# Kernel tuning notes

Hardware: AMD Instinct MI355X
Metric: run time of the kernel (lower is better)

The kernel has to match this reference:

```python
import jax, jax.numpy as jnp
import numpy as np

B, N, C = 2, 3136, 256
NUM_HEADS = 8
RADIUS = 3.0


def spatial_mask(H, W, radius):
    # [N, 2] pixel coordinates, then pairwise Euclidean distance mask
    yy, xx = jnp.meshgrid(jnp.arange(H), jnp.arange(W), indexing='ij')
    coords = jnp.stack([yy, xx], axis=-1).astype(jnp.float32).reshape(-1, 2)
    d2 = jnp.sum((coords[:, None, :] - coords[None, :, :]) ** 2, axis=-1)
    return jnp.where(d2 > radius * radius, -jnp.inf, 0.0)  # [N, N]


def setup_inputs() -> dict:
    key = jax.random.key(0)
    ks = jax.random.split(key, 7)
    w = 0.02
    return {
        'x': jax.random.normal(ks[0], (B, N, C), jnp.float32),
        'x_kv': jax.random.normal(ks[1], (B, N, C), jnp.float32),
        'Wq': jax.random.normal(ks[2], (C, C), jnp.float32) * w,
        'Wk': jax.random.normal(ks[3], (C, C), jnp.float32) * w,
        'Wv': jax.random.normal(ks[4], (C, C), jnp.float32) * w,
        'Wp': jax.random.normal(ks[5], (C, C), jnp.float32) * w,
        'bp': jnp.zeros((C,), jnp.float32),
    }


def reference(x, x_kv, Wq, Wk, Wv, Wp, bp):
    Bc, Nc, Cc = x.shape
    H = W = int(Nc ** 0.5)
    hd = Cc // NUM_HEADS
    scale = hd ** (-0.5)
    # torch Linear: y = x @ W.T ; split heads -> [B, h, N, hd]
    q = (x @ Wq.T).reshape(Bc, Nc, NUM_HEADS, hd).transpose(0, 2, 1, 3)
    k = (x_kv @ Wk.T).reshape(Bc, Nc, NUM_HEADS, hd).transpose(0, 2, 1, 3)
    v = (x_kv @ Wv.T).reshape(Bc, Nc, NUM_HEADS, hd).transpose(0, 2, 1, 3)
    attn = jnp.einsum('bhnd,bhmd->bhnm', q, k) * scale
    attn = attn + spatial_mask(H, W, RADIUS)[None, None, :, :]
    attn = jax.nn.softmax(attn, axis=-1)
    out = jnp.einsum('bhnm,bhmd->bhnd', attn, v)
    out = out.transpose(0, 2, 1, 3).reshape(Bc, Nc, Cc)
    return out @ Wp.T + bp
```

## Files before the change

### kernel.cpp

```cpp
#include <hip/hip_runtime.h>


typedef float  f32x4  __attribute__((ext_vector_type(4)));
typedef __bf16 bf16x8 __attribute__((ext_vector_type(8)));
typedef unsigned short u16x4 __attribute__((ext_vector_type(4)));
typedef unsigned short u16x8 __attribute__((ext_vector_type(8)));

#define Nn    3136
#define Cc    256
#define Mrows 6272
#define BNC   1605632
#define GRID56 56

__device__ __forceinline__ unsigned short f2bf(float f) {
    unsigned u = __builtin_bit_cast(unsigned, f);
    u += 0x7fffu + ((u >> 16) & 1u);
    return (unsigned short)(u >> 16);
}
__device__ __forceinline__ float bf2f(unsigned short h) {
    unsigned u = (unsigned)h << 16;
    return __builtin_bit_cast(float, u);
}

template<bool A_BF16, bool OUT_BF16>
__device__ __forceinline__ void gemm_body(
    const void* __restrict__ Ap, const float* __restrict__ W,
    const float* __restrict__ bias, void* __restrict__ Yv,
    int m0, int n0)
{
    constexpr int LDSW = 72;
    __shared__ unsigned short lA[64 * LDSW];
    __shared__ unsigned short lB[64 * LDSW];

    const int t    = threadIdx.x;
    const int lane = t & 63;
    const int wave = t >> 6;
    const int wm   = wave >> 1;
    const int wn   = wave & 1;
    const int srow = t >> 2;
    const int scol = (t & 3) * 16;
    const int fr   = lane & 15;
    const int fk   = (lane >> 4) * 8;

    f32x4 acc[2][2] = {};

    for (int k0 = 0; k0 < 256; k0 += 64) {
        u16x8 astage[2], bstage[2];
        if constexpr (A_BF16) {
            const unsigned short* A = (const unsigned short*)Ap;
            astage[0] = *reinterpret_cast<const u16x8*>(A + (size_t)(m0 + srow) * 256 + k0 + scol);
            astage[1] = *reinterpret_cast<const u16x8*>(A + (size_t)(m0 + srow) * 256 + k0 + scol + 8);
        } else {
            const float* A = (const float*)Ap;
            f32x4 a4[4];
#pragma unroll
            for (int j = 0; j < 4; ++j)
                a4[j] = *reinterpret_cast<const f32x4*>(A + (size_t)(m0 + srow) * 256 + k0 + scol + j * 4);
#pragma unroll
            for (int j = 0; j < 4; ++j)
#pragma unroll
                for (int e = 0; e < 4; ++e)
                    astage[j >> 1][(j & 1) * 4 + e] = f2bf(a4[j][e]);
        }
        {
            f32x4 b4[4];
#pragma unroll
            for (int j = 0; j < 4; ++j)
                b4[j] = *reinterpret_cast<const f32x4*>(W + (size_t)(n0 + srow) * 256 + k0 + scol + j * 4);
#pragma unroll
            for (int j = 0; j < 4; ++j)
#pragma unroll
                for (int e = 0; e < 4; ++e)
                    bstage[j >> 1][(j & 1) * 4 + e] = f2bf(b4[j][e]);
        }

        __syncthreads();
        *reinterpret_cast<u16x8*>(&lA[srow * LDSW + scol])     = astage[0];
        *reinterpret_cast<u16x8*>(&lA[srow * LDSW + scol + 8]) = astage[1];
        *reinterpret_cast<u16x8*>(&lB[srow * LDSW + scol])     = bstage[0];
        *reinterpret_cast<u16x8*>(&lB[srow * LDSW + scol + 8]) = bstage[1];
        __syncthreads();

        bf16x8 af[2][2], bfr[2][2];
#pragma unroll
        for (int i = 0; i < 2; ++i)
#pragma unroll
            for (int h = 0; h < 2; ++h) {
                af[i][h]  = *reinterpret_cast<const bf16x8*>(&lA[(wm * 32 + i * 16 + fr) * LDSW + h * 32 + fk]);
                bfr[i][h] = *reinterpret_cast<const bf16x8*>(&lB[(wn * 32 + i * 16 + fr) * LDSW + h * 32 + fk]);
            }
#pragma unroll
        for (int h = 0; h < 2; ++h)
#pragma unroll
            for (int i = 0; i < 2; ++i)
#pragma unroll
                for (int j = 0; j < 2; ++j)
                    acc[i][j] = __builtin_amdgcn_mfma_f32_16x16x32_bf16(af[i][h], bfr[j][h], acc[i][j], 0, 0, 0);
    }

#pragma unroll
    for (int i = 0; i < 2; ++i)
#pragma unroll
        for (int j = 0; j < 2; ++j) {
            int rbase = m0 + wm * 32 + i * 16 + (lane >> 4) * 4;
            int c     = n0 + wn * 32 + j * 16 + fr;
            if constexpr (OUT_BF16) {
                unsigned short* Y = (unsigned short*)Yv;
#pragma unroll
                for (int e = 0; e < 4; ++e)
                    Y[(size_t)(rbase + e) * 256 + c] = f2bf(acc[i][j][e]);
            } else {
                float* Y = (float*)Yv;
                float badd = bias[c];
#pragma unroll
                for (int e = 0; e < 4; ++e)
                    Y[(size_t)(rbase + e) * 256 + c] = acc[i][j][e] + badd;
            }
        }
}

__global__ __launch_bounds__(256) void gemm_qkv_kernel(
    const float* __restrict__ x, const float* __restrict__ xkv,
    const float* __restrict__ Wq, const float* __restrict__ Wk,
    const float* __restrict__ Wv,
    unsigned short* __restrict__ Qb, unsigned short* __restrict__ Kb,
    unsigned short* __restrict__ Vb)
{
    int z = blockIdx.z;
    const float* A = (z == 0) ? x : xkv;
    const float* W = (z == 0) ? Wq : (z == 1 ? Wk : Wv);
    unsigned short* Y = (z == 0) ? Qb : (z == 1 ? Kb : Vb);
    gemm_body<false, true>(A, W, nullptr, Y, blockIdx.x * 64, blockIdx.y * 64);
}

__global__ __launch_bounds__(256) void gemm_proj_kernel(
    const unsigned short* __restrict__ attb, const float* __restrict__ Wp,
    const float* __restrict__ bias, float* __restrict__ Y)
{
    gemm_body<true, false>(attb, Wp, bias, Y, blockIdx.x * 64, blockIdx.y * 64);
}

__global__ __launch_bounds__(256) void attn_local(
    const unsigned short* __restrict__ Q, const unsigned short* __restrict__ K,
    const unsigned short* __restrict__ V, unsigned short* __restrict__ outb)
{
    const int wave = threadIdx.x >> 6;
    const int lane = threadIdx.x & 63;
    const int q = blockIdx.x * 4 + wave;
    const int b = q / Nn;
    const int n = q - b * Nn;
    const int y = n / GRID56;
    const int x = n - y * GRID56;
    const float scale = 0.17677669529663687f;

    u16x4 qr = *reinterpret_cast<const u16x4*>(Q + (size_t)q * Cc + lane * 4);
    float q0 = bf2f(qr[0]), q1 = bf2f(qr[1]), q2 = bf2f(qr[2]), q3 = bf2f(qr[3]);

    float m_run = -INFINITY, l_run = 0.0f;
    f32x4 acc = {0.0f, 0.0f, 0.0f, 0.0f};

#pragma unroll
    for (int dy = -3; dy <= 3; ++dy) {
        int yy = y + dy;
        if ((unsigned)yy >= (unsigned)GRID56) continue;
        int R = (dy == 0) ? 3 : ((dy == 3 || dy == -3) ? 0 : 2);
#pragma unroll
        for (int dx = -3; dx <= 3; ++dx) {
            if (dx < -R || dx > R) continue;
            int xx = x + dx;
            if ((unsigned)xx >= (unsigned)GRID56) continue;
            int m = b * Nn + yy * GRID56 + xx;
            u16x4 kr = *reinterpret_cast<const u16x4*>(K + (size_t)m * Cc + lane * 4);
            u16x4 vr = *reinterpret_cast<const u16x4*>(V + (size_t)m * Cc + lane * 4);
            float p = q0 * bf2f(kr[0]) + q1 * bf2f(kr[1]) + q2 * bf2f(kr[2]) + q3 * bf2f(kr[3]);
            p += __shfl_xor(p, 1);
            p += __shfl_xor(p, 2);
            p += __shfl_xor(p, 4);
            float s = p * scale;
            float m_new = fmaxf(m_run, s);
            float corr = __expf(m_run - m_new);
            float pe   = __expf(s - m_new);
            l_run = l_run * corr + pe;
            acc[0] = acc[0] * corr + pe * bf2f(vr[0]);
            acc[1] = acc[1] * corr + pe * bf2f(vr[1]);
            acc[2] = acc[2] * corr + pe * bf2f(vr[2]);
            acc[3] = acc[3] * corr + pe * bf2f(vr[3]);
            m_run = m_new;
        }
    }
    float inv = 1.0f / l_run;
    u16x4 o;
    o[0] = f2bf(acc[0] * inv); o[1] = f2bf(acc[1] * inv);
    o[2] = f2bf(acc[2] * inv); o[3] = f2bf(acc[3] * inv);
    *reinterpret_cast<u16x4*>(outb + (size_t)q * Cc + lane * 4) = o;
}

extern "C" void kernel_launch(void* const* d_in, const int* in_sizes, int n_in,
                              void* d_out, int out_size, void* d_ws, size_t ws_size,
                              hipStream_t stream)
{
    const float* x   = (const float*)d_in[0];
    const float* xkv = (const float*)d_in[1];
    const float* Wq  = (const float*)d_in[2];
    const float* Wk  = (const float*)d_in[3];
    const float* Wv  = (const float*)d_in[4];
    const float* Wp  = (const float*)d_in[5];
    const float* bp  = (const float*)d_in[6];
    float* out = (float*)d_out;

    char* ws = (char*)d_ws;
    unsigned short* Qb   = (unsigned short*)ws; ws += (size_t)BNC * 2;
    unsigned short* Kb   = (unsigned short*)ws; ws += (size_t)BNC * 2;
    unsigned short* Vb   = (unsigned short*)ws; ws += (size_t)BNC * 2;
    unsigned short* attb = (unsigned short*)ws; ws += (size_t)BNC * 2;

    dim3 gqkv(Mrows / 64, Cc / 64, 3);
    gemm_qkv_kernel<<<gqkv, 256, 0, stream>>>(x, xkv, Wq, Wk, Wv, Qb, Kb, Vb);
    attn_local<<<Mrows / 4, 256, 0, stream>>>(Qb, Kb, Vb, attb);
    dim3 gproj(Mrows / 64, Cc / 64, 1);
    gemm_proj_kernel<<<gproj, 256, 0, stream>>>(attb, Wp, bp, out);
}
```

Measured before the change: 115.6 us.

## Enlarge GEMM tiles to 128x256 with 512-thread blocks covering full output width

The QKV and projection GEMMs now use 128-row by 256-column tiles with 8 waves, each computing a 64x64 sub-tile of 4x4 MFMAs. Each block covers the full output width, so A is read and converted from fp32 once per row instead of four times. The trade-off is far fewer blocks (49 per GEMM slice) on a many-CU GPU, more registers per thread and more LDS per block, which could leave the device underutilized.

```diff
diff --git a/kernel.cpp b/kernel.cpp
--- a/kernel.cpp
+++ b/kernel.cpp
@@ -25,37 +25,38 @@
 template<bool A_BF16, bool OUT_BF16>
 __device__ __forceinline__ void gemm_body(
     const void* __restrict__ Ap, const float* __restrict__ W,
-    const float* __restrict__ bias, void* __restrict__ Yv,
-    int m0, int n0)
+    const float* __restrict__ bias, void* __restrict__ Yv, int m0)
 {
     constexpr int LDSW = 72;
-    __shared__ unsigned short lA[64 * LDSW];
-    __shared__ unsigned short lB[64 * LDSW];
+    __shared__ unsigned short lA[128 * LDSW];
+    __shared__ unsigned short lB[256 * LDSW];
 
     const int t    = threadIdx.x;
     const int lane = t & 63;
     const int wave = t >> 6;
-    const int wm   = wave >> 1;
-    const int wn   = wave & 1;
-    const int srow = t >> 2;
-    const int scol = (t & 3) * 16;
+    const int wm   = wave >> 2;
+    const int wn   = wave & 3;
     const int fr   = lane & 15;
     const int fk   = (lane >> 4) * 8;
-
-    f32x4 acc[2][2] = {};
+    const int srowA = t >> 2;
+    const int scolA = (t & 3) * 16;
+    const int srowB = t >> 1;
+    const int scolB = (t & 1) * 32;
+
+    f32x4 acc[4][4] = {};
 
     for (int k0 = 0; k0 < 256; k0 += 64) {
-        u16x8 astage[2], bstage[2];
+        u16x8 astage[2], bstage[4];
         if constexpr (A_BF16) {
             const unsigned short* A = (const unsigned short*)Ap;
-            astage[0] = *reinterpret_cast<const u16x8*>(A + (size_t)(m0 + srow) * 256 + k0 + scol);
-            astage[1] = *reinterpret_cast<const u16x8*>(A + (size_t)(m0 + srow) * 256 + k0 + scol + 8);
+            astage[0] = *reinterpret_cast<const u16x8*>(A + (size_t)(m0 + srowA) * 256 + k0 + scolA);
+            astage[1] = *reinterpret_cast<const u16x8*>(A + (size_t)(m0 + srowA) * 256 + k0 + scolA + 8);
         } else {
             const float* A = (const float*)Ap;
             f32x4 a4[4];
 #pragma unroll
             for (int j = 0; j < 4; ++j)
-                a4[j] = *reinterpret_cast<const f32x4*>(A + (size_t)(m0 + srow) * 256 + k0 + scol + j * 4);
+                a4[j] = *reinterpret_cast<const f32x4*>(A + (size_t)(m0 + srowA) * 256 + k0 + scolA + j * 4);
 #pragma unroll
             for (int j = 0; j < 4; ++j)
 #pragma unroll
@@ -63,47 +64,48 @@
                     astage[j >> 1][(j & 1) * 4 + e] = f2bf(a4[j][e]);
         }
         {
-            f32x4 b4[4];
-#pragma unroll
-            for (int j = 0; j < 4; ++j)
-                b4[j] = *reinterpret_cast<const f32x4*>(W + (size_t)(n0 + srow) * 256 + k0 + scol + j * 4);
-#pragma unroll
-            for (int j = 0; j < 4; ++j)
+            f32x4 b4[8];
+#pragma unroll
+            for (int j = 0; j < 8; ++j)
+                b4[j] = *reinterpret_cast<const f32x4*>(W + (size_t)srowB * 256 + k0 + scolB + j * 4);
+#pragma unroll
+            for (int j = 0; j < 8; ++j)
 #pragma unroll
                 for (int e = 0; e < 4; ++e)
                     bstage[j >> 1][(j & 1) * 4 + e] = f2bf(b4[j][e]);
         }
 
         __syncthreads();
-        *reinterpret_cast<u16x8*>(&lA[srow * LDSW + scol])     = astage[0];
-        *reinterpret_cast<u16x8*>(&lA[srow * LDSW + scol + 8]) = astage[1];
-        *reinterpret_cast<u16x8*>(&lB[srow * LDSW + scol])     = bstage[0];
-        *reinterpret_cast<u16x8*>(&lB[srow * LDSW + scol + 8]) = bstage[1];
+        *reinterpret_cast<u16x8*>(&lA[srowA * LDSW + scolA])     = astage[0];
+        *reinterpret_cast<u16x8*>(&lA[srowA * LDSW + scolA + 8]) = astage[1];
+#pragma unroll
+        for (int j = 0; j < 4; ++j)
+            *reinterpret_cast<u16x8*>(&lB[srowB * LDSW + scolB + j * 8]) = bstage[j];
         __syncthreads();
 
-        bf16x8 af[2][2], bfr[2][2];
-#pragma unroll
-        for (int i = 0; i < 2; ++i)
+        bf16x8 af[4][2], bfr[4][2];
+#pragma unroll
+        for (int i = 0; i < 4; ++i)
 #pragma unroll
             for (int h = 0; h < 2; ++h) {
-                af[i][h]  = *reinterpret_cast<const bf16x8*>(&lA[(wm * 32 + i * 16 + fr) * LDSW + h * 32 + fk]);
-                bfr[i][h] = *reinterpret_cast<const bf16x8*>(&lB[(wn * 32 + i * 16 + fr) * LDSW + h * 32 + fk]);
+                af[i][h]  = *reinterpret_cast<const bf16x8*>(&lA[(wm * 64 + i * 16 + fr) * LDSW + h * 32 + fk]);
+                bfr[i][h] = *reinterpret_cast<const bf16x8*>(&lB[(wn * 64 + i * 16 + fr) * LDSW + h * 32 + fk]);
             }
 #pragma unroll
         for (int h = 0; h < 2; ++h)
 #pragma unroll
-            for (int i = 0; i < 2; ++i)
-#pragma unroll
-                for (int j = 0; j < 2; ++j)
+            for (int i = 0; i < 4; ++i)
+#pragma unroll
+                for (int j = 0; j < 4; ++j)
                     acc[i][j] = __builtin_amdgcn_mfma_f32_16x16x32_bf16(af[i][h], bfr[j][h], acc[i][j], 0, 0, 0);
     }
 
 #pragma unroll
-    for (int i = 0; i < 2; ++i)
-#pragma unroll
-        for (int j = 0; j < 2; ++j) {
-            int rbase = m0 + wm * 32 + i * 16 + (lane >> 4) * 4;
-            int c     = n0 + wn * 32 + j * 16 + fr;
+    for (int i = 0; i < 4; ++i)
+#pragma unroll
+        for (int j = 0; j < 4; ++j) {
+            int rbase = m0 + wm * 64 + i * 16 + (lane >> 4) * 4;
+            int c     = wn * 64 + j * 16 + fr;
             if constexpr (OUT_BF16) {
                 unsigned short* Y = (unsigned short*)Yv;
 #pragma unroll
@@ -119,7 +121,7 @@
         }
 }
 
-__global__ __launch_bounds__(256) void gemm_qkv_kernel(
+__global__ __launch_bounds__(512) void gemm_qkv_kernel(
     const float* __restrict__ x, const float* __restrict__ xkv,
     const float* __restrict__ Wq, const float* __restrict__ Wk,
     const float* __restrict__ Wv,
@@ -130,14 +132,14 @@
     const float* A = (z == 0) ? x : xkv;
     const float* W = (z == 0) ? Wq : (z == 1 ? Wk : Wv);
     unsigned short* Y = (z == 0) ? Qb : (z == 1 ? Kb : Vb);
-    gemm_body<false, true>(A, W, nullptr, Y, blockIdx.x * 64, blockIdx.y * 64);
-}
-
-__global__ __launch_bounds__(256) void gemm_proj_kernel(
+    gemm_body<false, true>(A, W, nullptr, Y, blockIdx.x * 128);
+}
+
+__global__ __launch_bounds__(512) void gemm_proj_kernel(
     const unsigned short* __restrict__ attb, const float* __restrict__ Wp,
     const float* __restrict__ bias, float* __restrict__ Y)
 {
-    gemm_body<true, false>(attb, Wp, bias, Y, blockIdx.x * 64, blockIdx.y * 64);
+    gemm_body<true, false>(attb, Wp, bias, Y, blockIdx.x * 128);
 }
 
 __global__ __launch_bounds__(256) void attn_local(
@@ -214,9 +216,8 @@
     unsigned short* Vb   = (unsigned short*)ws; ws += (size_t)BNC * 2;
     unsigned short* attb = (unsigned short*)ws; ws += (size_t)BNC * 2;
 
-    dim3 gqkv(Mrows / 64, Cc / 64, 3);
-    gemm_qkv_kernel<<<gqkv, 256, 0, stream>>>(x, xkv, Wq, Wk, Wv, Qb, Kb, Vb);
+    dim3 gqkv(Mrows / 128, 1, 3);
+    gemm_qkv_kernel<<<gqkv, 512, 0, stream>>>(x, xkv, Wq, Wk, Wv, Qb, Kb, Vb);
     attn_local<<<Mrows / 4, 256, 0, stream>>>(Qb, Kb, Vb, attb);
-    dim3 gproj(Mrows / 64, Cc / 64, 1);
-    gemm_proj_kernel<<<gproj, 256, 0, stream>>>(attb, Wp, bp, out);
-}
+    gemm_proj_kernel<<<Mrows / 128, 512, 0, stream>>>(attb, Wp, bp, out);
+}
```

Measured after the change: 125.4 us. 1.08x slower.

## Pre-convert weights to bf16 and double-buffer GEMM LDS tiles

Applied to the files above, without the earlier changes.

Adds a small kernel that converts all four weight matrices to bf16 once per call, so the GEMMs load bf16 weights directly instead of converting fp32 tiles in every block. The GEMM main loop now double-buffers LDS and prefetches the next K-stage into registers while the current one runs MFMA, which removes one barrier per iteration. It also replaces the manual rounding helpers with native __bf16 casts. The cost is one extra kernel launch, a little more workspace, and twice the LDS per block.

```diff
diff --git a/kernel.cpp b/kernel.cpp
--- a/kernel.cpp
+++ b/kernel.cpp
@@ -2,6 +2,7 @@
 
 
 typedef float  f32x4  __attribute__((ext_vector_type(4)));
+typedef __bf16 bf16x4 __attribute__((ext_vector_type(4)));
 typedef __bf16 bf16x8 __attribute__((ext_vector_type(8)));
 typedef unsigned short u16x4 __attribute__((ext_vector_type(4)));
 typedef unsigned short u16x8 __attribute__((ext_vector_type(8)));
@@ -10,27 +11,38 @@
 #define Cc    256
 #define Mrows 6272
 #define BNC   1605632
+#define CC    65536
 #define GRID56 56
 
-__device__ __forceinline__ unsigned short f2bf(float f) {
-    unsigned u = __builtin_bit_cast(unsigned, f);
-    u += 0x7fffu + ((u >> 16) & 1u);
-    return (unsigned short)(u >> 16);
-}
-__device__ __forceinline__ float bf2f(unsigned short h) {
-    unsigned u = (unsigned)h << 16;
-    return __builtin_bit_cast(float, u);
+__device__ __forceinline__ float bf2f(__bf16 h) { return (float)h; }
+
+__global__ __launch_bounds__(256) void convert_w(
+    const float* __restrict__ wq, const float* __restrict__ wk,
+    const float* __restrict__ wv, const float* __restrict__ wp,
+    __bf16* __restrict__ wqb, __bf16* __restrict__ wkb,
+    __bf16* __restrict__ wvb, __bf16* __restrict__ wpb)
+{
+    const int NW = CC / 4;
+    int i = blockIdx.x * blockDim.x + threadIdx.x;
+    int wsel = i >> 14;
+    int off  = i & (NW - 1);
+    const float* src = (wsel == 0) ? wq : (wsel == 1) ? wk : (wsel == 2) ? wv : wp;
+    __bf16* dst = (wsel == 0) ? wqb : (wsel == 1) ? wkb : (wsel == 2) ? wvb : wpb;
+    f32x4 v = *reinterpret_cast<const f32x4*>(src + (size_t)off * 4);
+    bf16x4 o;
+    o[0] = (__bf16)v[0]; o[1] = (__bf16)v[1]; o[2] = (__bf16)v[2]; o[3] = (__bf16)v[3];
+    *reinterpret_cast<bf16x4*>(dst + (size_t)off * 4) = o;
 }
 
 template<bool A_BF16, bool OUT_BF16>
 __device__ __forceinline__ void gemm_body(
-    const void* __restrict__ Ap, const float* __restrict__ W,
+    const void* __restrict__ Ap, const __bf16* __restrict__ Wb,
     const float* __restrict__ bias, void* __restrict__ Yv,
     int m0, int n0)
 {
     constexpr int LDSW = 72;
-    __shared__ unsigned short lA[64 * LDSW];
-    __shared__ unsigned short lB[64 * LDSW];
+    __shared__ __bf16 lA[2][64 * LDSW];
+    __shared__ __bf16 lB[2][64 * LDSW];
 
     const int t    = threadIdx.x;
     const int lane = t & 63;
@@ -44,12 +56,12 @@
 
     f32x4 acc[2][2] = {};
 
-    for (int k0 = 0; k0 < 256; k0 += 64) {
-        u16x8 astage[2], bstage[2];
+    bf16x8 ast[2], bst[2];
+    auto load_stage = [&](int k0) {
         if constexpr (A_BF16) {
-            const unsigned short* A = (const unsigned short*)Ap;
-            astage[0] = *reinterpret_cast<const u16x8*>(A + (size_t)(m0 + srow) * 256 + k0 + scol);
-            astage[1] = *reinterpret_cast<const u16x8*>(A + (size_t)(m0 + srow) * 256 + k0 + scol + 8);
+            const __bf16* A = (const __bf16*)Ap;
+            ast[0] = *reinterpret_cast<const bf16x8*>(A + (size_t)(m0 + srow) * 256 + k0 + scol);
+            ast[1] = *reinterpret_cast<const bf16x8*>(A + (size_t)(m0 + srow) * 256 + k0 + scol + 8);
         } else {
             const float* A = (const float*)Ap;
             f32x4 a4[4];
@@ -60,34 +72,30 @@
             for (int j = 0; j < 4; ++j)
 #pragma unroll
                 for (int e = 0; e < 4; ++e)
-                    astage[j >> 1][(j & 1) * 4 + e] = f2bf(a4[j][e]);
+                    ast[j >> 1][(j & 1) * 4 + e] = (__bf16)a4[j][e];
         }
-        {
-            f32x4 b4[4];
-#pragma unroll
-            for (int j = 0; j < 4; ++j)
-                b4[j] = *reinterpret_cast<const f32x4*>(W + (size_t)(n0 + srow) * 256 + k0 + scol + j * 4);
-#pragma unroll
-            for (int j = 0; j < 4; ++j)
-#pragma unroll
-                for (int e = 0; e < 4; ++e)
-                    bstage[j >> 1][(j & 1) * 4 + e] = f2bf(b4[j][e]);
-        }
-
+        bst[0] = *reinterpret_cast<const bf16x8*>(Wb + (size_t)(n0 + srow) * 256 + k0 + scol);
+        bst[1] = *reinterpret_cast<const bf16x8*>(Wb + (size_t)(n0 + srow) * 256 + k0 + scol + 8);
+    };
+
+    load_stage(0);
+    int p = 0;
+#pragma unroll
+    for (int it = 0; it < 4; ++it) {
+        *reinterpret_cast<bf16x8*>(&lA[p][srow * LDSW + scol])     = ast[0];
+        *reinterpret_cast<bf16x8*>(&lA[p][srow * LDSW + scol + 8]) = ast[1];
+        *reinterpret_cast<bf16x8*>(&lB[p][srow * LDSW + scol])     = bst[0];
+        *reinterpret_cast<bf16x8*>(&lB[p][srow * LDSW + scol + 8]) = bst[1];
         __syncthreads();
-        *reinterpret_cast<u16x8*>(&lA[srow * LDSW + scol])     = astage[0];
-        *reinterpret_cast<u16x8*>(&lA[srow * LDSW + scol + 8]) = astage[1];
-        *reinterpret_cast<u16x8*>(&lB[srow * LDSW + scol])     = bstage[0];
-        *reinterpret_cast<u16x8*>(&lB[srow * LDSW + scol + 8]) = bstage[1];
-        __syncthreads();
+        if (it < 3) load_stage((it + 1) * 64);
 
         bf16x8 af[2][2], bfr[2][2];
 #pragma unroll
         for (int i = 0; i < 2; ++i)
 #pragma unroll
             for (int h = 0; h < 2; ++h) {
-                af[i][h]  = *reinterpret_cast<const bf16x8*>(&lA[(wm * 32 + i * 16 + fr) * LDSW + h * 32 + fk]);
-                bfr[i][h] = *reinterpret_cast<const bf16x8*>(&lB[(wn * 32 + i * 16 + fr) * LDSW + h * 32 + fk]);
+                af[i][h]  = *reinterpret_cast<const bf16x8*>(&lA[p][(wm * 32 + i * 16 + fr) * LDSW + h * 32 + fk]);
+                bfr[i][h] = *reinterpret_cast<const bf16x8*>(&lB[p][(wn * 32 + i * 16 + fr) * LDSW + h * 32 + fk]);
             }
 #pragma unroll
         for (int h = 0; h < 2; ++h)
@@ -96,6 +104,7 @@
 #pragma unroll
                 for (int j = 0; j < 2; ++j)
                     acc[i][j] = __builtin_amdgcn_mfma_f32_16x16x32_bf16(af[i][h], bfr[j][h], acc[i][j], 0, 0, 0);
+        p ^= 1;
     }
 
 #pragma unroll
@@ -105,10 +114,10 @@
             int rbase = m0 + wm * 32 + i * 16 + (lane >> 4) * 4;
             int c     = n0 + wn * 32 + j * 16 + fr;
             if constexpr (OUT_BF16) {
-                unsigned short* Y = (unsigned short*)Yv;
+                __bf16* Y = (__bf16*)Yv;
 #pragma unroll
                 for (int e = 0; e < 4; ++e)
-                    Y[(size_t)(rbase + e) * 256 + c] = f2bf(acc[i][j][e]);
+                    Y[(size_t)(rbase + e) * 256 + c] = (__bf16)acc[i][j][e];
             } else {
                 float* Y = (float*)Yv;
                 float badd = bias[c];
@@ -121,28 +130,27 @@
 
 __global__ __launch_bounds__(256) void gemm_qkv_kernel(
     const float* __restrict__ x, const float* __restrict__ xkv,
-    const float* __restrict__ Wq, const float* __restrict__ Wk,
-    const float* __restrict__ Wv,
-    unsigned short* __restrict__ Qb, unsigned short* __restrict__ Kb,
-    unsigned short* __restrict__ Vb)
+    const __bf16* __restrict__ wqb, const __bf16* __restrict__ wkb,
+    const __bf16* __restrict__ wvb,
+    __bf16* __restrict__ Qb, __bf16* __restrict__ Kb, __bf16* __restrict__ Vb)
 {
     int z = blockIdx.z;
     const float* A = (z == 0) ? x : xkv;
-    const float* W = (z == 0) ? Wq : (z == 1 ? Wk : Wv);
-    unsigned short* Y = (z == 0) ? Qb : (z == 1 ? Kb : Vb);
+    const __bf16* W = (z == 0) ? wqb : (z == 1 ? wkb : wvb);
+    __bf16* Y = (z == 0) ? Qb : (z == 1 ? Kb : Vb);
     gemm_body<false, true>(A, W, nullptr, Y, blockIdx.x * 64, blockIdx.y * 64);
 }
 
 __global__ __launch_bounds__(256) void gemm_proj_kernel(
-    const unsigned short* __restrict__ attb, const float* __restrict__ Wp,
+    const __bf16* __restrict__ attb, const __bf16* __restrict__ wpb,
     const float* __restrict__ bias, float* __restrict__ Y)
 {
-    gemm_body<true, false>(attb, Wp, bias, Y, blockIdx.x * 64, blockIdx.y * 64);
+    gemm_body<true, false>(attb, wpb, bias, Y, blockIdx.x * 64, blockIdx.y * 64);
 }
 
 __global__ __launch_bounds__(256) void attn_local(
-    const unsigned short* __restrict__ Q, const unsigned short* __restrict__ K,
-    const unsigned short* __restrict__ V, unsigned short* __restrict__ outb)
+    const __bf16* __restrict__ Q, const __bf16* __restrict__ K,
+    const __bf16* __restrict__ V, __bf16* __restrict__ outb)
 {
     const int wave = threadIdx.x >> 6;
     const int lane = threadIdx.x & 63;
@@ -153,7 +161,7 @@
     const int x = n - y * GRID56;
     const float scale = 0.17677669529663687f;
 
-    u16x4 qr = *reinterpret_cast<const u16x4*>(Q + (size_t)q * Cc + lane * 4);
+    bf16x4 qr = *reinterpret_cast<const bf16x4*>(Q + (size_t)q * Cc + lane * 4);
     float q0 = bf2f(qr[0]), q1 = bf2f(qr[1]), q2 = bf2f(qr[2]), q3 = bf2f(qr[3]);
 
     float m_run = -INFINITY, l_run = 0.0f;
@@ -170,13 +178,13 @@
             int xx = x + dx;
             if ((unsigned)xx >= (unsigned)GRID56) continue;
             int m = b * Nn + yy * GRID56 + xx;
-            u16x4 kr = *reinterpret_cast<const u16x4*>(K + (size_t)m * Cc + lane * 4);
-            u16x4 vr = *reinterpret_cast<const u16x4*>(V + (size_t)m * Cc + lane * 4);
-            float p = q0 * bf2f(kr[0]) + q1 * bf2f(kr[1]) + q2 * bf2f(kr[2]) + q3 * bf2f(kr[3]);
-            p += __shfl_xor(p, 1);
-            p += __shfl_xor(p, 2);
-            p += __shfl_xor(p, 4);
-            float s = p * scale;
+            bf16x4 kr = *reinterpret_cast<const bf16x4*>(K + (size_t)m * Cc + lane * 4);
+            bf16x4 vr = *reinterpret_cast<const bf16x4*>(V + (size_t)m * Cc + lane * 4);
+            float pdot = q0 * bf2f(kr[0]) + q1 * bf2f(kr[1]) + q2 * bf2f(kr[2]) + q3 * bf2f(kr[3]);
+            pdot += __shfl_xor(pdot, 1);
+            pdot += __shfl_xor(pdot, 2);
+            pdot += __shfl_xor(pdot, 4);
+            float s = pdot * scale;
             float m_new = fmaxf(m_run, s);
             float corr = __expf(m_run - m_new);
             float pe   = __expf(s - m_new);
@@ -189,10 +197,10 @@
         }
     }
     float inv = 1.0f / l_run;
-    u16x4 o;
-    o[0] = f2bf(acc[0] * inv); o[1] = f2bf(acc[1] * inv);
-    o[2] = f2bf(acc[2] * inv); o[3] = f2bf(acc[3] * inv);
-    *reinterpret_cast<u16x4*>(outb + (size_t)q * Cc + lane * 4) = o;
+    bf16x4 o;
+    o[0] = (__bf16)(acc[0] * inv); o[1] = (__bf16)(acc[1] * inv);
+    o[2] = (__bf16)(acc[2] * inv); o[3] = (__bf16)(acc[3] * inv);
+    *reinterpret_cast<bf16x4*>(outb + (size_t)q * Cc + lane * 4) = o;
 }
 
 extern "C" void kernel_launch(void* const* d_in, const int* in_sizes, int n_in,
@@ -209,14 +217,19 @@
     float* out = (float*)d_out;
 
     char* ws = (char*)d_ws;
-    unsigned short* Qb   = (unsigned short*)ws; ws += (size_t)BNC * 2;
-    unsigned short* Kb   = (unsigned short*)ws; ws += (size_t)BNC * 2;
-    unsigned short* Vb   = (unsigned short*)ws; ws += (size_t)BNC * 2;
-    unsigned short* attb = (unsigned short*)ws; ws += (size_t)BNC * 2;
-
+    __bf16* Qb   = (__bf16*)ws; ws += (size_t)BNC * 2;
+    __bf16* Kb   = (__bf16*)ws; ws += (size_t)BNC * 2;
+    __bf16* Vb   = (__bf16*)ws; ws += (size_t)BNC * 2;
+    __bf16* attb = (__bf16*)ws; ws += (size_t)BNC * 2;
+    __bf16* wqb  = (__bf16*)ws; ws += (size_t)CC * 2;
+    __bf16* wkb  = (__bf16*)ws; ws += (size_t)CC * 2;
+    __bf16* wvb  = (__bf16*)ws; ws += (size_t)CC * 2;
+    __bf16* wpb  = (__bf16*)ws; ws += (size_t)CC * 2;
+
+    convert_w<<<256, 256, 0, stream>>>(Wq, Wk, Wv, Wp, wqb, wkb, wvb, wpb);
     dim3 gqkv(Mrows / 64, Cc / 64, 3);
-    gemm_qkv_kernel<<<gqkv, 256, 0, stream>>>(x, xkv, Wq, Wk, Wv, Qb, Kb, Vb);
+    gemm_qkv_kernel<<<gqkv, 256, 0, stream>>>(x, xkv, wqb, wkb, wvb, Qb, Kb, Vb);
     attn_local<<<Mrows / 4, 256, 0, stream>>>(Qb, Kb, Vb, attb);
     dim3 gproj(Mrows / 64, Cc / 64, 1);
-    gemm_proj_kernel<<<gproj, 256, 0, stream>>>(attb, Wp, bp, out);
-}
+    gemm_proj_kernel<<<gproj, 256, 0, stream>>>(attb, wpb, bp, out);
+}
```

After: 113.8 us. No clear change (-1.5%).
